# Kernel optimization log

Measured on AMD Instinct MI355X. Metric: run time of the kernel, lower is better.

## Reference

```python
import math
import jax, jax.numpy as jnp
import numpy as np

B, N, D, H, L = 8, 1024, 512, 8, 6
HD = D // H
FREQ = 256
K_LORENTZ = 1.0


def lorentz_projx(x, k=K_LORENTZ):
    # geoopt Lorentz.projx: x0 = sqrt(k + ||x_space||^2)
    space = x[..., 1:]
    x0 = jnp.sqrt(k + jnp.sum(space * space, axis=-1, keepdims=True))
    return jnp.concatenate([x0, space], axis=-1)


def layernorm(x, eps=1e-6):
    m = jnp.mean(x, axis=-1, keepdims=True)
    v = jnp.mean((x - m) ** 2, axis=-1, keepdims=True)
    return (x - m) / jnp.sqrt(v + eps)


def make_pe(n, d):
    pos = np.arange(n, dtype=np.float32)[:, None]
    div = np.exp(np.arange(0, d, 2, dtype=np.float32) * (-math.log(10000.0) / d))
    pe = np.zeros((n, d), dtype=np.float32)
    pe[:, 0::2] = np.sin(pos * div)
    pe[:, 1::2] = np.cos(pos * div)
    return jnp.asarray(pe)


def setup_inputs() -> dict:
    key = jax.random.key(0)
    ks = jax.random.split(key, 20)
    s = 0.02
    inp = {
        "t": jax.random.uniform(ks[0], (B,), jnp.float32) * 1000.0,
        "x": jax.random.normal(ks[1], (B, N, D), jnp.float32),
        "mask": jnp.ones((B, N), jnp.float32),
        "pe": make_pe(N, D),
        # timestep embedder MLP (weights stored [in,out])
        "tw1": jax.random.normal(ks[2], (FREQ, D), jnp.float32) * s,
        "tb1": jnp.zeros((D,), jnp.float32),
        "tw2": jax.random.normal(ks[3], (D, D), jnp.float32) * s,
        "tb2": jnp.zeros((D,), jnp.float32),
        # per-layer params stacked over L
        "Wq": jax.random.normal(ks[4], (L, D, D), jnp.float32) * s,
        "bq": jnp.zeros((L, D), jnp.float32),
        "Wk": jax.random.normal(ks[5], (L, D, D), jnp.float32) * s,
        "bk": jnp.zeros((L, D), jnp.float32),
        "Wv": jax.random.normal(ks[6], (L, D, D), jnp.float32) * s,
        "bv": jnp.zeros((L, D), jnp.float32),
        "W1": jax.random.normal(ks[7], (L, D, 4 * D), jnp.float32) * s,
        "b1": jnp.zeros((L, 4 * D), jnp.float32),
        "W2": jax.random.normal(ks[8], (L, 4 * D, D), jnp.float32) * s,
        "b2": jnp.zeros((L, D), jnp.float32),
        "Wada": jax.random.normal(ks[9], (L, D, 6 * D), jnp.float32) * s,
        "bada": jnp.zeros((L, 6 * D), jnp.float32),
    }
    return inp


def timestep_embedding(t, dim=FREQ, max_period=10000.0):
    half = dim // 2
    freqs = jnp.exp(-math.log(max_period) * jnp.arange(half, dtype=jnp.float32) / half)
    args = t[:, None] * freqs[None]
    return jnp.concatenate([jnp.cos(args), jnp.sin(args)], axis=-1)  # [B, dim]


def attention(h, mask, Wq, bq, Wk, bk, Wv, bv):
    # h: [B,N,D], mask: [B,N]
    q = (h @ Wq + bq).reshape(B, N, H, HD).transpose(0, 2, 1, 3)
    k = (h @ Wk + bk).reshape(B, N, H, HD).transpose(0, 2, 1, 3)
    v = (h @ Wv + bv).reshape(B, N, H, HD).transpose(0, 2, 1, 3)
    scores = jnp.einsum("bhqd,bhkd->bhqk", q, k) / math.sqrt(HD)
    # faithful quirk: valid positions get +1 added, invalid get -10000
    mm = jnp.einsum("bi,bj->bij", mask, mask)[:, None]  # [B,1,N,N]
    mm = jnp.where(mm == 0, -10000.0, mm)
    scores = scores + mm
    probs = jax.nn.softmax(scores, axis=-1)
    ctx = jnp.einsum("bhqk,bhkd->bhqd", probs, v)
    return ctx.transpose(0, 2, 1, 3).reshape(B, N, D)


def reference(t, x, mask, pe, tw1, tb1, tw2, tb2, Wq, bq, Wk, bk, Wv, bv,
              W1, b1, W2, b2, Wada, bada):
    # z = x + PositionalEncoding(x) = 2*x + pe
    z = x + (x + pe[None])
    # timestep embedder
    c = timestep_embedding(t) @ tw1 + tb1
    c = jax.nn.silu(c) @ tw2 + tb2  # [B, D]
    for i in range(L):
        ada = jax.nn.silu(c) @ Wada[i] + bada[i]  # [B, 6D]
        sh_msa, sc_msa, g_msa, sh_mlp, sc_mlp, g_mlp = jnp.split(ada, 6, axis=-1)
        h = layernorm(z) * (1.0 + sc_msa[:, None]) + sh_msa[:, None]
        z = z + g_msa[:, None] * attention(h, mask, Wq[i], bq[i], Wk[i], bk[i], Wv[i], bv[i])
        z = lorentz_projx(z)
        h = layernorm(z) * (1.0 + sc_mlp[:, None]) + sh_mlp[:, None]
        m = jax.nn.gelu(h @ W1[i] + b1[i], approximate=True) @ W2[i] + b2[i]
        z = z + g_mlp[:, None] * m
        z = lorentz_projx(z)
    z = lorentz_projx(z)
    return jnp.where(mask[:, :, None] != 0, z, 0.0)
```

## Files before the change

kernel.cpp:

```cpp
#include <hip/hip_runtime.h>
#include <hip/hip_bf16.h>
#include <math.h>

#define NTOK 1024
#define DMODEL 512
#define NHEAD 8
#define HDIM 64
#define BATCH 8
#define NLAYER 6
#define ROWS (BATCH*NTOK)
#define QKVSTR 1536
#define LOG2E 1.44269504f

typedef __attribute__((ext_vector_type(8))) short bf16x8;
typedef __attribute__((ext_vector_type(4))) float f32x4;
typedef unsigned short ushort_t;


__device__ __forceinline__ float silu_f(float x) { return x / (1.f + expf(-x)); }

__device__ __forceinline__ float gelu_tanh_f(float x) {
    float x3 = x * x * x;
    float y2 = 1.5957691216057308f * (x + 0.044715f * x3);
    float e = __builtin_amdgcn_exp2f(-y2 * LOG2E);
    return x / (1.f + e);
}

__device__ __forceinline__ unsigned short f2bf(float x) {
    __hip_bfloat16 b = __float2bfloat16(x);
    return *reinterpret_cast<unsigned short*>(&b);
}

__device__ __forceinline__ float bf2f(unsigned short u) {
    union { float f; unsigned v; } c;
    c.v = (unsigned)u << 16;
    return c.f;
}

__device__ __forceinline__ float wave_sum(float v) {
    #pragma unroll
    for (int o = 1; o < 64; o <<= 1) v += __shfl_xor(v, o);
    return v;
}


__global__ __launch_bounds__(256) void init_z_kernel(const float* __restrict__ x,
                                                     const float* __restrict__ pe,
                                                     float* __restrict__ z) {
    int i = blockIdx.x * 256 + threadIdx.x;
    const int C4 = DMODEL / 4;
    int row = i / C4;
    int col4 = i - row * C4;
    int n = row & (NTOK - 1);
    float4 xv = ((const float4*)x)[i];
    float4 pv = ((const float4*)pe)[n * C4 + col4];
    float4 o;
    o.x = 2.f * xv.x + pv.x;
    o.y = 2.f * xv.y + pv.y;
    o.z = 2.f * xv.z + pv.z;
    o.w = 2.f * xv.w + pv.w;
    ((float4*)z)[i] = o;
}

__global__ void temb_kernel(const float* __restrict__ t, float* __restrict__ temb) {
    int b = blockIdx.x;
    int j = threadIdx.x;
    float f = expf(-9.210340371976184f * (float)j / 128.f);
    float a = t[b] * f;
    temb[b * 256 + j] = cosf(a);
    temb[b * 256 + 128 + j] = sinf(a);
}

__global__ void zero512(float* __restrict__ p) {
    p[blockIdx.x * 256 + threadIdx.x] = 0.f;
}

__global__ __launch_bounds__(256) void skinny_part(const float* __restrict__ A,
                                                   const float* __restrict__ W,
                                                   float* __restrict__ part,
                                                   int K, int N, int NL) {
    __shared__ float Als[8][128];
    const int l = blockIdx.z;
    const int n = blockIdx.x * 256 + threadIdx.x;
    const int kc = blockIdx.y;
    const int kbase = kc * 128;
    for (int i = threadIdx.x; i < 8 * 128; i += 256) {
        int b = i >> 7, k = i & 127;
        Als[b][k] = A[b * K + kbase + k];
    }
    __syncthreads();
    float acc[8] = {};
    const float* wp = W + (size_t)l * K * N + (size_t)kbase * N + n;
    for (int k = 0; k < 128; k += 4) {
        float w0 = wp[0];
        float w1 = wp[N];
        float w2 = wp[2 * N];
        float w3 = wp[3 * N];
        wp += 4 * (size_t)N;
        #pragma unroll
        for (int b = 0; b < 8; b++)
            acc[b] += Als[b][k] * w0 + Als[b][k + 1] * w1 + Als[b][k + 2] * w2 + Als[b][k + 3] * w3;
    }
    #pragma unroll
    for (int b = 0; b < 8; b++)
        part[((size_t)kc * 8 + b) * NL + (size_t)l * N + n] = acc[b];
}

template<int ACT>
__global__ __launch_bounds__(256) void skinny_reduce(const float* __restrict__ part,
                                                     const float* __restrict__ bias,
                                                     float* __restrict__ out,
                                                     int KC, int N, int NL) {
    int i = blockIdx.x * 256 + threadIdx.x;
    if (i >= 8 * NL) return;
    int b = i / NL, n = i - b * NL;
    float s = bias[n];
    for (int kc = 0; kc < KC; kc++) s += part[((size_t)kc * 8 + b) * NL + n];
    if (ACT == 1) s = silu_f(s);
    int l = n / N, nl = n - l * N;
    out[((size_t)l * 8 + b) * N + nl] = s;
}

__global__ __launch_bounds__(256) void transp_all(const float* __restrict__ Wq,
                                                  const float* __restrict__ Wk,
                                                  const float* __restrict__ Wv,
                                                  const float* __restrict__ W1,
                                                  const float* __restrict__ W2,
                                                  ushort_t* __restrict__ wqkv_t,
                                                  ushort_t* __restrict__ w1_t,
                                                  ushort_t* __restrict__ w2_t) {
    __shared__ float tile[32][33];
    int blk = blockIdx.x;
    const float* src; ushort_t* dst; int K, N, k0, n0;
    if (blk < 768) {
        int zz = blk >> 8, rem = blk & 255;
        k0 = (rem >> 4) * 32; n0 = (rem & 15) * 32;
        src = zz == 0 ? Wq : (zz == 1 ? Wk : Wv);
        dst = wqkv_t + zz * 512 * 512;
        K = 512; N = 512;
    } else if (blk < 1792) {
        int rem = blk - 768;
        n0 = (rem & 63) * 32; k0 = (rem >> 6) * 32;
        src = W1; dst = w1_t; K = 512; N = 2048;
    } else {
        int rem = blk - 1792;
        n0 = (rem & 15) * 32; k0 = (rem >> 4) * 32;
        src = W2; dst = w2_t; K = 2048; N = 512;
    }
    int c = threadIdx.x & 31, r8 = threadIdx.x >> 5;
    #pragma unroll
    for (int i = 0; i < 4; i++) {
        int r = r8 + i * 8;
        tile[r][c] = src[(size_t)(k0 + r) * N + n0 + c];
    }
    __syncthreads();
    #pragma unroll
    for (int i = 0; i < 4; i++) {
        int rr = r8 + i * 8;
        dst[(size_t)(n0 + rr) * K + k0 + c] = f2bf(tile[c][rr]);
    }
}

__global__ void pack_bias(const float* __restrict__ bq, const float* __restrict__ bk,
                          const float* __restrict__ bv, float* __restrict__ bqkv) {
    int idx = blockIdx.x * 256 + threadIdx.x;
    if (idx >= NLAYER * QKVSTR) return;
    int l = idx / QKVSTR, n = idx - l * QKVSTR;
    float v = (n < 512) ? bq[l * 512 + n] : (n < 1024) ? bk[l * 512 + n - 512] : bv[l * 512 + n - 1024];
    bqkv[idx] = v;
}

template<int ACT, int OUTBF, int QPRESCALE, int SPLITK>
__global__ __launch_bounds__(256) void mfma_gemm(const ushort_t* __restrict__ A,
                                                 const ushort_t* __restrict__ Bt,
                                                 const float* __restrict__ bias,
                                                 void* __restrict__ Cout,
                                                 int M, int N, int K) {
    __shared__ ushort_t smem[4 * 128 * 64];
    const int tid = threadIdx.x;
    const int lane = tid & 63, wv = tid >> 6;
    const int wm = (wv >> 1) * 64, wn = (wv & 1) * 64;
    const int lrow = lane & 15, lk = lane >> 4;
    const int m0 = blockIdx.x * 128, n0 = blockIdx.y * 128;
    const int srow = lane >> 3;
    const int qp = lane & 7;
    const int ql = qp ^ srow;

    int Keff = K;
    if (SPLITK) {
        Keff = K >> 1;
        const size_t koff = (size_t)blockIdx.z * Keff;
        A += koff;
        Bt += koff;
        Cout = (void*)((ushort_t*)Cout + (size_t)blockIdx.z * M * N);
    }

    f32x4 acc[4][4];
    #pragma unroll
    for (int i = 0; i < 4; i++)
        #pragma unroll
        for (int j = 0; j < 4; j++) {
            f32x4 zz = {0.f, 0.f, 0.f, 0.f};
            acc[i][j] = zz;
        }

    const int nK = Keff >> 6;

    auto STAGE = [&](int p, int ks) {
        const int k0 = ks << 6;
        ushort_t* Ad = smem + p * 8192;
        ushort_t* Bd = smem + 16384 + p * 8192;
        #pragma unroll
        for (int it = 0; it < 4; it++) {
            int chunk = wv * 4 + it;
            int row = chunk * 8 + srow;
            const ushort_t* srcA = A + (size_t)(m0 + row) * K + k0 + ql * 8;
            const ushort_t* srcB = Bt + (size_t)(n0 + row) * K + k0 + ql * 8;
            __builtin_amdgcn_global_load_lds((const __attribute__((address_space(1))) void*)srcA,
                                             (__attribute__((address_space(3))) void*)(Ad + chunk * 512),
                                             16, 0, 0);
            __builtin_amdgcn_global_load_lds((const __attribute__((address_space(1))) void*)srcB,
                                             (__attribute__((address_space(3))) void*)(Bd + chunk * 512),
                                             16, 0, 0);
        }
    };

    STAGE(0, 0);
    int cur = 0;
    for (int ks = 0; ks < nK; ks++) {
        if (ks + 1 < nK) {
            STAGE(cur ^ 1, ks + 1);
            asm volatile("s_waitcnt vmcnt(8)" ::: "memory");
        } else {
            asm volatile("s_waitcnt vmcnt(0)" ::: "memory");
        }
        __builtin_amdgcn_s_barrier();
        asm volatile("" ::: "memory");

        const ushort_t* Ab = smem + cur * 8192;
        const ushort_t* Bb = smem + 16384 + cur * 8192;
        #pragma unroll
        for (int kk = 0; kk < 2; kk++) {
            bf16x8 af[4], bfr[4];
            #pragma unroll
            for (int f = 0; f < 4; f++) {
                int ar = wm + f * 16 + lrow;
                af[f] = *(const bf16x8*)(Ab + ar * 64 + (((kk * 4 + lk) ^ (ar & 7)) << 3));
                int br = wn + f * 16 + lrow;
                bfr[f] = *(const bf16x8*)(Bb + br * 64 + (((kk * 4 + lk) ^ (br & 7)) << 3));
            }
            #pragma unroll
            for (int i = 0; i < 4; i++)
                #pragma unroll
                for (int j = 0; j < 4; j++)
                    acc[i][j] = __builtin_amdgcn_mfma_f32_16x16x32_bf16(af[i], bfr[j], acc[i][j], 0, 0, 0);
        }
        asm volatile("" ::: "memory");
        __builtin_amdgcn_s_barrier();
        cur ^= 1;
    }

    if (OUTBF) {
        __syncthreads();
        #pragma unroll
        for (int j = 0; j < 4; j++) {
            int coll = wn + j * 16 + lrow;
            float bcol = bias[n0 + coll];
            #pragma unroll
            for (int i = 0; i < 4; i++) {
                #pragma unroll
                for (int r = 0; r < 4; r++) {
                    int rowl = wm + i * 16 + lk * 4 + r;
                    float v = acc[i][j][r] + bcol;
                    if (ACT == 1) v = gelu_tanh_f(v);
                    if (QPRESCALE && (n0 + coll) < 512) v *= 0.125f * LOG2E;
                    smem[rowl * 136 + coll] = f2bf(v);
                }
            }
        }
        __syncthreads();
        ushort_t* Co = (ushort_t*)Cout;
        #pragma unroll
        for (int pass = 0; pass < 8; pass++) {
            int rowl = pass * 16 + (tid >> 4);
            int cseg = (tid & 15) * 8;
            uint4 vv = *(const uint4*)(smem + rowl * 136 + cseg);
            *(uint4*)(Co + (size_t)(m0 + rowl) * N + n0 + cseg) = vv;
        }
    } else {
        #pragma unroll
        for (int j = 0; j < 4; j++) {
            int col = n0 + wn + j * 16 + lrow;
            float bcol = bias[col];
            #pragma unroll
            for (int i = 0; i < 4; i++)
                #pragma unroll
                for (int r = 0; r < 4; r++) {
                    int row = m0 + wm + i * 16 + lk * 4 + r;
                    float v = acc[i][j][r] + bcol;
                    if (ACT == 1) v = gelu_tanh_f(v);
                    ((float*)Cout)[(size_t)row * N + col] = v;
                }
        }
    }
}


__global__ __launch_bounds__(256) void ln_mod_kernel(const float* __restrict__ z,
                                                     const float* __restrict__ ada,
                                                     ushort_t* __restrict__ out,
                                                     int sh_off, int sc_off) {
    int lane = threadIdx.x & 63;
    int row = blockIdx.x * 4 + (threadIdx.x >> 6);
    int b = row >> 10;
    const float4* zr = (const float4*)(z + (size_t)row * DMODEL);
    float4 va = zr[lane * 2], vb = zr[lane * 2 + 1];
    float s = va.x + va.y + va.z + va.w + vb.x + vb.y + vb.z + vb.w;
    float mean = wave_sum(s) * (1.f / DMODEL);
    float d0 = va.x - mean, d1 = va.y - mean, d2 = va.z - mean, d3 = va.w - mean;
    float d4 = vb.x - mean, d5 = vb.y - mean, d6 = vb.z - mean, d7 = vb.w - mean;
    float ssq = d0*d0 + d1*d1 + d2*d2 + d3*d3 + d4*d4 + d5*d5 + d6*d6 + d7*d7;
    float rstd = rsqrtf(wave_sum(ssq) * (1.f / DMODEL) + 1e-6f);
    const float* ab = ada + b * (6 * DMODEL);
    const float4* scp = (const float4*)(ab + sc_off);
    const float4* shp = (const float4*)(ab + sh_off);
    float4 sca = scp[lane * 2], scb = scp[lane * 2 + 1];
    float4 sha = shp[lane * 2], shb = shp[lane * 2 + 1];
    uint4 pk;
    pk.x = (unsigned)f2bf(d0 * rstd * (1.f + sca.x) + sha.x) |
           ((unsigned)f2bf(d1 * rstd * (1.f + sca.y) + sha.y) << 16);
    pk.y = (unsigned)f2bf(d2 * rstd * (1.f + sca.z) + sha.z) |
           ((unsigned)f2bf(d3 * rstd * (1.f + sca.w) + sha.w) << 16);
    pk.z = (unsigned)f2bf(d4 * rstd * (1.f + scb.x) + shb.x) |
           ((unsigned)f2bf(d5 * rstd * (1.f + scb.y) + shb.y) << 16);
    pk.w = (unsigned)f2bf(d6 * rstd * (1.f + scb.z) + shb.z) |
           ((unsigned)f2bf(d7 * rstd * (1.f + scb.w) + shb.w) << 16);
    ((uint4*)(out + (size_t)row * DMODEL))[lane] = pk;
}

template<int TWO>
__global__ __launch_bounds__(256) void resid_ln_kernel(float* __restrict__ z,
                                                       const ushort_t* __restrict__ add,
                                                       const ushort_t* __restrict__ add2,
                                                       const float* __restrict__ abias,
                                                       const float* __restrict__ adaG, int g_off,
                                                       const float* __restrict__ adaLN, int sh_off, int sc_off,
                                                       ushort_t* __restrict__ out) {
    int lane = threadIdx.x & 63;
    int row = blockIdx.x * 4 + (threadIdx.x >> 6);
    int b = row >> 10;
    float4* zr = (float4*)(z + (size_t)row * DMODEL);
    float4 va = zr[lane * 2], vb = zr[lane * 2 + 1];
    uint4 a4 = ((const uint4*)(add + (size_t)row * DMODEL))[lane];
    const float4* gp = (const float4*)(adaG + b * (6 * DMODEL) + g_off);
    float4 ga = gp[lane * 2], gb = gp[lane * 2 + 1];
    const ushort_t* e = (const ushort_t*)&a4;
    float av[8];
    #pragma unroll
    for (int i = 0; i < 8; i++) av[i] = bf2f(e[i]);
    if (TWO) {
        uint4 a42 = ((const uint4*)(add2 + (size_t)row * DMODEL))[lane];
        const ushort_t* e2 = (const ushort_t*)&a42;
        float4 ba = ((const float4*)abias)[lane * 2];
        float4 bb = ((const float4*)abias)[lane * 2 + 1];
        av[0] += bf2f(e2[0]) + ba.x; av[1] += bf2f(e2[1]) + ba.y;
        av[2] += bf2f(e2[2]) + ba.z; av[3] += bf2f(e2[3]) + ba.w;
        av[4] += bf2f(e2[4]) + bb.x; av[5] += bf2f(e2[5]) + bb.y;
        av[6] += bf2f(e2[6]) + bb.z; av[7] += bf2f(e2[7]) + bb.w;
    }
    va.x += ga.x * av[0]; va.y += ga.y * av[1];
    va.z += ga.z * av[2]; va.w += ga.w * av[3];
    vb.x += gb.x * av[4]; vb.y += gb.y * av[5];
    vb.z += gb.z * av[6]; vb.w += gb.w * av[7];
    float ssq = va.x*va.x + va.y*va.y + va.z*va.z + va.w*va.w
              + vb.x*vb.x + vb.y*vb.y + vb.z*vb.z + vb.w*vb.w;
    if (lane == 0) ssq -= va.x * va.x;
    float tot = wave_sum(ssq);
    if (lane == 0) va.x = sqrtf(1.f + tot);
    zr[lane * 2] = va; zr[lane * 2 + 1] = vb;
    float s = va.x + va.y + va.z + va.w + vb.x + vb.y + vb.z + vb.w;
    float mean = wave_sum(s) * (1.f / DMODEL);
    float d0 = va.x - mean, d1 = va.y - mean, d2 = va.z - mean, d3 = va.w - mean;
    float d4 = vb.x - mean, d5 = vb.y - mean, d6 = vb.z - mean, d7 = vb.w - mean;
    float sq2 = d0*d0 + d1*d1 + d2*d2 + d3*d3 + d4*d4 + d5*d5 + d6*d6 + d7*d7;
    float rstd = rsqrtf(wave_sum(sq2) * (1.f / DMODEL) + 1e-6f);
    const float* ab = adaLN + b * (6 * DMODEL);
    const float4* scp = (const float4*)(ab + sc_off);
    const float4* shp = (const float4*)(ab + sh_off);
    float4 sca = scp[lane * 2], scb = scp[lane * 2 + 1];
    float4 sha = shp[lane * 2], shb = shp[lane * 2 + 1];
    uint4 pk;
    pk.x = (unsigned)f2bf(d0 * rstd * (1.f + sca.x) + sha.x) |
           ((unsigned)f2bf(d1 * rstd * (1.f + sca.y) + sha.y) << 16);
    pk.y = (unsigned)f2bf(d2 * rstd * (1.f + sca.z) + sha.z) |
           ((unsigned)f2bf(d3 * rstd * (1.f + sca.w) + sha.w) << 16);
    pk.z = (unsigned)f2bf(d4 * rstd * (1.f + scb.x) + shb.x) |
           ((unsigned)f2bf(d5 * rstd * (1.f + scb.y) + shb.y) << 16);
    pk.w = (unsigned)f2bf(d6 * rstd * (1.f + scb.z) + shb.z) |
           ((unsigned)f2bf(d7 * rstd * (1.f + scb.w) + shb.w) << 16);
    ((uint4*)(out + (size_t)row * DMODEL))[lane] = pk;
}

__global__ __launch_bounds__(256) void resid_final_kernel(const float* __restrict__ z,
                                                          const ushort_t* __restrict__ add,
                                                          const ushort_t* __restrict__ add2,
                                                          const float* __restrict__ abias,
                                                          const float* __restrict__ adaG, int g_off,
                                                          const float* __restrict__ mask,
                                                          float* __restrict__ out) {
    int lane = threadIdx.x & 63;
    int row = blockIdx.x * 4 + (threadIdx.x >> 6);
    int b = row >> 10;
    const float4* zr = (const float4*)(z + (size_t)row * DMODEL);
    float4 va = zr[lane * 2], vb = zr[lane * 2 + 1];
    uint4 a4 = ((const uint4*)(add + (size_t)row * DMODEL))[lane];
    uint4 a42 = ((const uint4*)(add2 + (size_t)row * DMODEL))[lane];
    const float4* gp = (const float4*)(adaG + b * (6 * DMODEL) + g_off);
    float4 ga = gp[lane * 2], gb = gp[lane * 2 + 1];
    const ushort_t* e = (const ushort_t*)&a4;
    const ushort_t* e2 = (const ushort_t*)&a42;
    float4 ba = ((const float4*)abias)[lane * 2];
    float4 bb = ((const float4*)abias)[lane * 2 + 1];
    va.x += ga.x * (bf2f(e[0]) + bf2f(e2[0]) + ba.x);
    va.y += ga.y * (bf2f(e[1]) + bf2f(e2[1]) + ba.y);
    va.z += ga.z * (bf2f(e[2]) + bf2f(e2[2]) + ba.z);
    va.w += ga.w * (bf2f(e[3]) + bf2f(e2[3]) + ba.w);
    vb.x += gb.x * (bf2f(e[4]) + bf2f(e2[4]) + bb.x);
    vb.y += gb.y * (bf2f(e[5]) + bf2f(e2[5]) + bb.y);
    vb.z += gb.z * (bf2f(e[6]) + bf2f(e2[6]) + bb.z);
    vb.w += gb.w * (bf2f(e[7]) + bf2f(e2[7]) + bb.w);
    float ssq = va.x*va.x + va.y*va.y + va.z*va.z + va.w*va.w
              + vb.x*vb.x + vb.y*vb.y + vb.z*vb.z + vb.w*vb.w;
    if (lane == 0) ssq -= va.x * va.x;
    float tot = wave_sum(ssq);
    if (lane == 0) va.x = sqrtf(1.f + tot);
    float m = mask[row];
    if (m == 0.f) {
        va.x = va.y = va.z = va.w = 0.f;
        vb.x = vb.y = vb.z = vb.w = 0.f;
    }
    float4* orow = (float4*)(out + (size_t)row * DMODEL);
    orow[lane * 2] = va; orow[lane * 2 + 1] = vb;
}

__global__ __launch_bounds__(512) void flash_attn_mfma(const ushort_t* __restrict__ qkv,
                                                       const float* __restrict__ mask,
                                                       ushort_t* __restrict__ ctx) {
    __shared__ ushort_t Kls[64 * 64];
    __shared__ ushort_t Vt[64 * 64];
    __shared__ ushort_t Pls[8][16 * 64];
    __shared__ float Mall[NTOK];

    const int tid = threadIdx.x;
    const int lane = tid & 63, w = tid >> 6;
    const int c = lane & 15, g = lane >> 4;
    const int bh = blockIdx.x;
    const int q0 = blockIdx.y * 128;
    const int b = bh >> 3, h = bh & 7;

    const ushort_t* qptr = qkv + (size_t)(b * NTOK + q0 + w * 16 + c) * QKVSTR + h * HDIM + g * 8;
    bf16x8 aq0 = *(const bf16x8*)(qptr);
    bf16x8 aq1 = *(const bf16x8*)(qptr + 32);

    const float mq = mask[b * NTOK + q0 + w * 16 + c];

    #pragma unroll
    for (int i = 0; i < 2; i++) Mall[tid + i * 512] = mask[b * NTOK + tid + i * 512];

    f32x4 o[4];
    #pragma unroll
    for (int j = 0; j < 4; j++) { f32x4 zz = {0.f,0.f,0.f,0.f}; o[j] = zz; }
    float l_run = 0.f;

    const int srow = lane >> 3, qp = lane & 7, ql = qp ^ srow;
    const int kp = tid & 31, dg = tid >> 5;

    char* Pw = (char*)&Pls[w][0];
    const int cswz = (c & 7) << 4;

    for (int kt = 0; kt < NTOK / 64; kt++) {
        const int k0 = kt * 64;
        __syncthreads();
        {
            int row = w * 8 + srow;
            const ushort_t* src = qkv + (size_t)(b * NTOK + k0 + row) * QKVSTR + 512 + h * HDIM + ql * 8;
            __builtin_amdgcn_global_load_lds((const __attribute__((address_space(1))) void*)src,
                                             (__attribute__((address_space(3))) void*)(Kls + w * 512),
                                             16, 0, 0);
        }
        {
            const ushort_t* v0 = qkv + (size_t)(b * NTOK + k0 + 2 * kp) * QKVSTR + 1024 + h * HDIM + dg * 4;
            uint2 r0 = *(const uint2*)v0;
            uint2 r1 = *(const uint2*)(v0 + QKVSTR);
            const ushort_t* e0 = (const ushort_t*)&r0;
            const ushort_t* e1 = (const ushort_t*)&r1;
            unsigned* VtU = (unsigned*)Vt;
            #pragma unroll
            for (int i = 0; i < 4; i++) {
                int d = dg * 4 + i;
                unsigned pk = (unsigned)e0[i] | ((unsigned)e1[i] << 16);
                VtU[d * 32 + (((kp >> 2) ^ (d & 7)) << 2) + (kp & 3)] = pk;
            }
        }
        __syncthreads();

        f32x4 s[4];
        #pragma unroll
        for (int j = 0; j < 4; j++) { f32x4 zz = {0.f,0.f,0.f,0.f}; s[j] = zz; }
        __builtin_amdgcn_s_setprio(1);
        #pragma unroll
        for (int j = 0; j < 4; j++) {
            int row = j * 16 + c;
            bf16x8 ak0 = *(const bf16x8*)(Kls + row * 64 + ((g ^ (row & 7)) << 3));
            bf16x8 ak1 = *(const bf16x8*)(Kls + row * 64 + (((4 + g) ^ (row & 7)) << 3));
            s[j] = __builtin_amdgcn_mfma_f32_16x16x32_bf16(ak0, aq0, s[j], 0, 0, 0);
            s[j] = __builtin_amdgcn_mfma_f32_16x16x32_bf16(ak1, aq1, s[j], 0, 0, 0);
        }
        __builtin_amdgcn_s_setprio(0);

        #pragma unroll
        for (int j = 0; j < 4; j++) {
            float4 mk4 = *(const float4*)&Mall[k0 + j * 16 + 4 * g];
            const float* mkp = (const float*)&mk4;
            float p[4];
            #pragma unroll
            for (int r = 0; r < 4; r++) {
                float mm = mq * mkp[r];
                float sv = s[j][r] + (mm == 0.f ? -14427.0f : mm * LOG2E);
                p[r] = exp2f(sv);
                l_run += p[r];
            }
            uint2 pk2;
            pk2.x = (unsigned)f2bf(p[0]) | ((unsigned)f2bf(p[1]) << 16);
            pk2.y = (unsigned)f2bf(p[2]) | ((unsigned)f2bf(p[3]) << 16);
            *(uint2*)(Pw + c * 128 + ((j * 32 + g * 8) ^ cswz)) = pk2;
        }

        __builtin_amdgcn_s_setprio(1);
        #pragma unroll
        for (int kk = 0; kk < 2; kk++) {
            bf16x8 pa = *(const bf16x8*)(Pw + c * 128 + ((kk * 64 + g * 16) ^ cswz));
            #pragma unroll
            for (int j = 0; j < 4; j++) {
                int vr = j * 16 + c;
                bf16x8 bv = *(const bf16x8*)(Vt + vr * 64 + (((kk * 4 + g) ^ (vr & 7)) << 3));
                o[j] = __builtin_amdgcn_mfma_f32_16x16x32_bf16(pa, bv, o[j], 0, 0, 0);
            }
        }
        __builtin_amdgcn_s_setprio(0);
    }

    l_run += __shfl_xor(l_run, 16);
    l_run += __shfl_xor(l_run, 32);

    float invr[4];
    #pragma unroll
    for (int r = 0; r < 4; r++) invr[r] = 1.f / __shfl(l_run, (g << 4) + 4 * g + r);
    #pragma unroll
    for (int r = 0; r < 4; r++) {
        size_t row = (size_t)(b * NTOK + q0 + w * 16 + 4 * g + r) * DMODEL + h * HDIM;
        #pragma unroll
        for (int j = 0; j < 4; j++)
            ctx[row + j * 16 + c] = f2bf(o[j][r] * invr[r]);
    }
}


extern "C" void kernel_launch(void* const* d_in, const int* in_sizes, int n_in,
                              void* d_out, int out_size, void* d_ws, size_t ws_size,
                              hipStream_t stream) {
    const float* t    = (const float*)d_in[0];
    const float* x    = (const float*)d_in[1];
    const float* mask = (const float*)d_in[2];
    const float* pe   = (const float*)d_in[3];
    const float* tw1  = (const float*)d_in[4];
    const float* tb1  = (const float*)d_in[5];
    const float* tw2  = (const float*)d_in[6];
    const float* tb2  = (const float*)d_in[7];
    const float* Wq   = (const float*)d_in[8];
    const float* bq   = (const float*)d_in[9];
    const float* Wk   = (const float*)d_in[10];
    const float* bk   = (const float*)d_in[11];
    const float* Wv   = (const float*)d_in[12];
    const float* bv   = (const float*)d_in[13];
    const float* W1   = (const float*)d_in[14];
    const float* b1   = (const float*)d_in[15];
    const float* W2   = (const float*)d_in[16];
    const float* b2   = (const float*)d_in[17];
    const float* Wada = (const float*)d_in[18];
    const float* bada = (const float*)d_in[19];
    float* out = (float*)d_out;

    float* z      = (float*)d_ws;
    ushort_t* cxb = (ushort_t*)(z + (size_t)ROWS * DMODEL);
    ushort_t* cxb2 = cxb + (size_t)ROWS * DMODEL;
    ushort_t* qkv = cxb2 + (size_t)ROWS * DMODEL;
    ushort_t* mid = qkv;
    ushort_t* hb  = qkv + (size_t)ROWS * 2048;
    ushort_t* wqkv_t = hb + (size_t)ROWS * DMODEL;
    ushort_t* w1_t   = wqkv_t + 1536 * 512;
    ushort_t* w2_t   = w1_t + 2048 * 512;
    float* bqkv  = (float*)(w2_t + 512 * 2048);
    float* fzero = bqkv + NLAYER * QKVSTR;
    float* temb  = fzero + 512;
    float* cmid  = temb + BATCH * 256;
    float* scs   = cmid + BATCH * DMODEL;
    float* part  = scs + BATCH * DMODEL;
    float* ada_all = part + 4 * 8 * (NLAYER * 3072);

    init_z_kernel<<<ROWS * DMODEL / 4 / 256, 256, 0, stream>>>(x, pe, z);
    temb_kernel<<<BATCH, 128, 0, stream>>>(t, temb);
    pack_bias<<<(NLAYER * QKVSTR + 255) / 256, 256, 0, stream>>>(bq, bk, bv, bqkv);
    zero512<<<2, 256, 0, stream>>>(fzero);

    skinny_part<<<dim3(2, 2, 1), 256, 0, stream>>>(temb, tw1, part, 256, 512, 512);
    skinny_reduce<1><<<16, 256, 0, stream>>>(part, tb1, cmid, 2, 512, 512);
    skinny_part<<<dim3(2, 4, 1), 256, 0, stream>>>(cmid, tw2, part, 512, 512, 512);
    skinny_reduce<1><<<16, 256, 0, stream>>>(part, tb2, scs, 4, 512, 512);
    skinny_part<<<dim3(12, 4, NLAYER), 256, 0, stream>>>(scs, Wada, part, 512, 3072, NLAYER * 3072);
    skinny_reduce<0><<<(8 * NLAYER * 3072 + 255) / 256, 256, 0, stream>>>(
        part, bada, ada_all, 4, 3072, NLAYER * 3072);

    dim3 gqkv(ROWS / 128, QKVSTR / 128);
    dim3 gmlp1(ROWS / 128, 2048 / 128);
    dim3 gmlp2(ROWS / 128, DMODEL / 128, 2);
    dim3 ga(BATCH * NHEAD, NTOK / 128);

    ln_mod_kernel<<<ROWS / 4, 256, 0, stream>>>(z, ada_all, hb, 0, 512);

    for (int i = 0; i < NLAYER; i++) {
        const float* ada = ada_all + (size_t)i * 8 * 3072;

        transp_all<<<2816, 256, 0, stream>>>(Wq + (size_t)i * 512 * 512,
                                             Wk + (size_t)i * 512 * 512,
                                             Wv + (size_t)i * 512 * 512,
                                             W1 + (size_t)i * 512 * 2048,
                                             W2 + (size_t)i * 2048 * 512,
                                             wqkv_t, w1_t, w2_t);

        mfma_gemm<0, 1, 1, 0><<<gqkv, 256, 0, stream>>>(hb, wqkv_t, bqkv + i * QKVSTR, qkv,
                                                        ROWS, QKVSTR, DMODEL);

        flash_attn_mfma<<<ga, 512, 0, stream>>>(qkv, mask, cxb);

        resid_ln_kernel<0><<<ROWS / 4, 256, 0, stream>>>(z, cxb, nullptr, nullptr,
                                                         ada, 2 * DMODEL,
                                                         ada, 3 * DMODEL, 4 * DMODEL, hb);

        mfma_gemm<1, 1, 0, 0><<<gmlp1, 256, 0, stream>>>(hb, w1_t, b1 + (size_t)i * 4 * DMODEL, mid,
                                                         ROWS, 4 * DMODEL, DMODEL);
        mfma_gemm<0, 1, 0, 1><<<gmlp2, 256, 0, stream>>>(mid, w2_t, fzero, cxb,
                                                         ROWS, DMODEL, 4 * DMODEL);

        if (i < NLAYER - 1) {
            const float* adan = ada_all + (size_t)(i + 1) * 8 * 3072;
            resid_ln_kernel<1><<<ROWS / 4, 256, 0, stream>>>(z, cxb, cxb2, b2 + (size_t)i * DMODEL,
                                                             ada, 5 * DMODEL,
                                                             adan, 0, 512, hb);
        } else {
            resid_final_kernel<<<ROWS / 4, 256, 0, stream>>>(z, cxb, cxb2, b2 + (size_t)i * DMODEL,
                                                             ada, 5 * DMODEL, mask, out);
        }
    }
}
```

Measured before the change: 913.9 us.

## Double-buffer K/V tiles in flash attention to overlap loads with MFMA

K and V shared-memory tiles become double-buffered. The next tile's K (async global-to-LDS) and V (register) loads are issued before the current tile's QK and PV MFMAs. The V transpose-write goes into the other buffer after compute, which leaves one barrier per iteration instead of two. This hides global load latency behind compute, at the cost of doubled K/V LDS and extra live registers for the prefetched V.

```diff
diff --git a/kernel.cpp b/kernel.cpp
--- a/kernel.cpp
+++ b/kernel.cpp
@@ -446,8 +446,8 @@
 __global__ __launch_bounds__(512) void flash_attn_mfma(const ushort_t* __restrict__ qkv,
                                                        const float* __restrict__ mask,
                                                        ushort_t* __restrict__ ctx) {
-    __shared__ ushort_t Kls[64 * 64];
-    __shared__ ushort_t Vt[64 * 64];
+    __shared__ ushort_t Kls[2][64 * 64];
+    __shared__ ushort_t Vt[2][64 * 64];
     __shared__ ushort_t Pls[8][16 * 64];
     __shared__ float Mall[NTOK];
 
@@ -478,32 +478,50 @@
     char* Pw = (char*)&Pls[w][0];
     const int cswz = (c & 7) << 4;
 
+    auto KSTAGE = [&](int buf, int k0) {
+        int row = w * 8 + srow;
+        const ushort_t* src = qkv + (size_t)(b * NTOK + k0 + row) * QKVSTR + 512 + h * HDIM + ql * 8;
+        __builtin_amdgcn_global_load_lds((const __attribute__((address_space(1))) void*)src,
+                                         (__attribute__((address_space(3))) void*)(&Kls[buf][w * 512]),
+                                         16, 0, 0);
+    };
+    auto VLOAD = [&](int k0, uint2& r0, uint2& r1) {
+        const ushort_t* v0 = qkv + (size_t)(b * NTOK + k0 + 2 * kp) * QKVSTR + 1024 + h * HDIM + dg * 4;
+        r0 = *(const uint2*)v0;
+        r1 = *(const uint2*)(v0 + QKVSTR);
+    };
+    auto VWRITE = [&](int buf, uint2 r0, uint2 r1) {
+        const ushort_t* e0 = (const ushort_t*)&r0;
+        const ushort_t* e1 = (const ushort_t*)&r1;
+        unsigned* VtU = (unsigned*)&Vt[buf][0];
+        #pragma unroll
+        for (int i = 0; i < 4; i++) {
+            int d = dg * 4 + i;
+            unsigned pk = (unsigned)e0[i] | ((unsigned)e1[i] << 16);
+            VtU[d * 32 + (((kp >> 2) ^ (d & 7)) << 2) + (kp & 3)] = pk;
+        }
+    };
+
+    {
+        KSTAGE(0, 0);
+        uint2 r0, r1;
+        VLOAD(0, r0, r1);
+        asm volatile("s_waitcnt vmcnt(0)" ::: "memory");
+        VWRITE(0, r0, r1);
+    }
+    __syncthreads();
+
+    int cur = 0;
     for (int kt = 0; kt < NTOK / 64; kt++) {
         const int k0 = kt * 64;
-        __syncthreads();
-        {
-            int row = w * 8 + srow;
-            const ushort_t* src = qkv + (size_t)(b * NTOK + k0 + row) * QKVSTR + 512 + h * HDIM + ql * 8;
-            __builtin_amdgcn_global_load_lds((const __attribute__((address_space(1))) void*)src,
-                                             (__attribute__((address_space(3))) void*)(Kls + w * 512),
-                                             16, 0, 0);
-        }
-        {
-            const ushort_t* v0 = qkv + (size_t)(b * NTOK + k0 + 2 * kp) * QKVSTR + 1024 + h * HDIM + dg * 4;
-            uint2 r0 = *(const uint2*)v0;
-            uint2 r1 = *(const uint2*)(v0 + QKVSTR);
-            const ushort_t* e0 = (const ushort_t*)&r0;
-            const ushort_t* e1 = (const ushort_t*)&r1;
-            unsigned* VtU = (unsigned*)Vt;
-            #pragma unroll
-            for (int i = 0; i < 4; i++) {
-                int d = dg * 4 + i;
-                unsigned pk = (unsigned)e0[i] | ((unsigned)e1[i] << 16);
-                VtU[d * 32 + (((kp >> 2) ^ (d & 7)) << 2) + (kp & 3)] = pk;
-            }
-        }
-        __syncthreads();
-
+        const bool hasnxt = (kt + 1) < NTOK / 64;
+        uint2 vr0, vr1;
+        if (hasnxt) {
+            KSTAGE(cur ^ 1, k0 + 64);
+            VLOAD(k0 + 64, vr0, vr1);
+        }
+
+        const ushort_t* Kb = &Kls[cur][0];
         f32x4 s[4];
         #pragma unroll
         for (int j = 0; j < 4; j++) { f32x4 zz = {0.f,0.f,0.f,0.f}; s[j] = zz; }
@@ -511,8 +529,8 @@
         #pragma unroll
         for (int j = 0; j < 4; j++) {
             int row = j * 16 + c;
-            bf16x8 ak0 = *(const bf16x8*)(Kls + row * 64 + ((g ^ (row & 7)) << 3));
-            bf16x8 ak1 = *(const bf16x8*)(Kls + row * 64 + (((4 + g) ^ (row & 7)) << 3));
+            bf16x8 ak0 = *(const bf16x8*)(Kb + row * 64 + ((g ^ (row & 7)) << 3));
+            bf16x8 ak1 = *(const bf16x8*)(Kb + row * 64 + (((4 + g) ^ (row & 7)) << 3));
             s[j] = __builtin_amdgcn_mfma_f32_16x16x32_bf16(ak0, aq0, s[j], 0, 0, 0);
             s[j] = __builtin_amdgcn_mfma_f32_16x16x32_bf16(ak1, aq1, s[j], 0, 0, 0);
         }
@@ -536,6 +554,7 @@
             *(uint2*)(Pw + c * 128 + ((j * 32 + g * 8) ^ cswz)) = pk2;
         }
 
+        const ushort_t* Vb = &Vt[cur][0];
         __builtin_amdgcn_s_setprio(1);
         #pragma unroll
         for (int kk = 0; kk < 2; kk++) {
@@ -543,11 +562,18 @@
             #pragma unroll
             for (int j = 0; j < 4; j++) {
                 int vr = j * 16 + c;
-                bf16x8 bv = *(const bf16x8*)(Vt + vr * 64 + (((kk * 4 + g) ^ (vr & 7)) << 3));
+                bf16x8 bv = *(const bf16x8*)(Vb + vr * 64 + (((kk * 4 + g) ^ (vr & 7)) << 3));
                 o[j] = __builtin_amdgcn_mfma_f32_16x16x32_bf16(pa, bv, o[j], 0, 0, 0);
             }
         }
         __builtin_amdgcn_s_setprio(0);
+
+        if (hasnxt) {
+            asm volatile("s_waitcnt vmcnt(0)" ::: "memory");
+            VWRITE(cur ^ 1, vr0, vr1);
+        }
+        __syncthreads();
+        cur ^= 1;
     }
 
     l_run += __shfl_xor(l_run, 16);
```

After: 939.9 us. 2.8% more time.
